# Optimization experiments

Measured on AMD Instinct MI355X. Metric: run time of the kernel, lower is better.

## Reference

```python
import jax, jax.numpy as jnp
import numpy as np

N_NODES = 50000
N_EDGES = 250000
DIMS = [300, 1024, 512, 256, 128, 2048]
NEG_SLOPE = 0.01  # F.leaky_relu default


def setup_inputs() -> dict:
    key = jax.random.key(0)
    ks = jax.random.split(key, 12)
    x = jax.random.normal(ks[0], (N_NODES, DIMS[0]), dtype=jnp.float32)
    src = jax.random.randint(ks[1], (N_EDGES,), 0, N_NODES)
    dst = jax.random.randint(ks[2], (N_EDGES,), 0, N_NODES)
    edge_index = jnp.stack([src, dst]).astype(jnp.int64)
    inp = {"x": x, "edge_index": edge_index}
    for i in range(5):
        fi, fo = DIMS[i], DIMS[i + 1]
        scale = 1.0 / np.sqrt(fi)
        inp[f"W{i+1}"] = jax.random.uniform(ks[3 + i], (fi, fo), dtype=jnp.float32, minval=-scale, maxval=scale)
        inp[f"b{i+1}"] = jnp.zeros((fo,), dtype=jnp.float32)
    return inp


def _graph_conv(x, W, b, src, dst, dinv_out, dinv_in):
    # DGL GraphConv with norm='both': D_in^{-1/2} A D_out^{-1/2} X W + b
    # per-node scalar norm commutes with the linear map, so apply W first
    # (cheaper to gather/scatter in the smaller of in/out dims; math identical)
    h = (x * dinv_out[:, None]) @ W                      # [N, out]
    agg = jax.ops.segment_sum(h[src], dst, num_segments=N_NODES)  # SpMM
    return agg * dinv_in[:, None] + b


def reference(x, edge_index, W1, b1, W2, b2, W3, b3, W4, b4, W5, b5):
    src, dst = edge_index[0], edge_index[1]
    ones = jnp.ones((N_EDGES,), dtype=x.dtype)
    out_deg = jax.ops.segment_sum(ones, src, num_segments=N_NODES)
    in_deg = jax.ops.segment_sum(ones, dst, num_segments=N_NODES)
    dinv_out = jax.lax.rsqrt(jnp.maximum(out_deg, 1.0))
    dinv_in = jax.lax.rsqrt(jnp.maximum(in_deg, 1.0))

    h = _graph_conv(x, W1, b1, src, dst, dinv_out, dinv_in)
    h = jax.nn.leaky_relu(h, NEG_SLOPE)
    h = _graph_conv(h, W2, b2, src, dst, dinv_out, dinv_in)
    h = jax.nn.leaky_relu(h, NEG_SLOPE)
    h = _graph_conv(h, W3, b3, src, dst, dinv_out, dinv_in)
    h = jax.nn.leaky_relu(h, NEG_SLOPE)
    h = _graph_conv(h, W4, b4, src, dst, dinv_out, dinv_in)
    h = jax.nn.leaky_relu(h, NEG_SLOPE)
    h = _graph_conv(h, W5, b5, src, dst, dinv_out, dinv_in)
    return h
```

## Files before the change

kernel.cpp:

```cpp
#include <hip/hip_runtime.h>

#define N_NODES 50000

typedef __attribute__((ext_vector_type(8))) short short8v;
typedef __attribute__((ext_vector_type(4))) float f32x4;
typedef unsigned int u32;
typedef unsigned short u16;

__device__ inline u16 bf16_rn(float a) {
    u32 u = __float_as_uint(a);
    return (u16)((u + 0x7FFFu + ((u >> 16) & 1u)) >> 16);
}
__device__ inline void bf16_split(float a, u16& h, u16& l) {
    h = bf16_rn(a);
    float hf = __uint_as_float(((u32)h) << 16);
    l = bf16_rn(a - hf);
}


__global__ void degree_kernel(const int* __restrict__ ei,
                              int* __restrict__ deg_out, int* __restrict__ deg_in, int E) {
    int e = blockIdx.x * blockDim.x + threadIdx.x;
    if (e >= E) return;
    int s = ei[e];
    int d = ei[E + e];
    if (s >= 0 && s < N_NODES) atomicAdd(&deg_out[s], 1);
    if (d >= 0 && d < N_NODES) atomicAdd(&deg_in[d], 1);
}

__global__ void dinv_kernel(const int* __restrict__ deg_out, const int* __restrict__ deg_in,
                            float* __restrict__ dinv_out, float* __restrict__ dinv_in, int n) {
    int v = blockIdx.x * blockDim.x + threadIdx.x;
    if (v >= n) return;
    dinv_out[v] = rsqrtf((float)max(deg_out[v], 1));
    dinv_in[v]  = rsqrtf((float)max(deg_in[v], 1));
}

__global__ void scan_kernel(const int* __restrict__ deg, int* __restrict__ row_start, int n) {
    __shared__ int sdata[1024];
    __shared__ int carry;
    int tid = threadIdx.x;
    if (tid == 0) { carry = 0; row_start[0] = 0; }
    __syncthreads();
    for (int base = 0; base < n; base += 1024) {
        int i = base + tid;
        int v = (i < n) ? deg[i] : 0;
        sdata[tid] = v;
        __syncthreads();
        for (int off = 1; off < 1024; off <<= 1) {
            int t = (tid >= off) ? sdata[tid - off] : 0;
            __syncthreads();
            sdata[tid] += t;
            __syncthreads();
        }
        if (i < n) row_start[i + 1] = carry + sdata[tid];
        __syncthreads();
        if (tid == 0) carry += sdata[1023];
        __syncthreads();
    }
}

__global__ void fill_kernel(const int* __restrict__ ei, const int* __restrict__ row_start,
                            int* __restrict__ fill_cnt, int* __restrict__ csr_src, int E) {
    int e = blockIdx.x * blockDim.x + threadIdx.x;
    if (e >= E) return;
    int s = ei[e];
    int d = ei[E + e];
    if (d < 0 || d >= N_NODES) return;
    int pos = row_start[d] + atomicAdd(&fill_cnt[d], 1);
    csr_src[pos] = s;
}


__global__ __launch_bounds__(256) void wsplit_kernel(
    const float* __restrict__ W, u16* __restrict__ Thi, u16* __restrict__ Tlo,
    int K, int Kp, int N)
{
    __shared__ float Ts[32][73];
    int tid = threadIdx.x;
    int k0 = blockIdx.x * 32, n0 = blockIdx.y * 64;
    int kk = tid >> 3, nn = (tid & 7) * 8;
    float4 v0 = make_float4(0.f, 0.f, 0.f, 0.f), v1 = v0;
    if (k0 + kk < K) {
        const float* p = W + (size_t)(k0 + kk) * N + n0 + nn;
        v0 = *reinterpret_cast<const float4*>(p);
        v1 = *reinterpret_cast<const float4*>(p + 4);
    }
    Ts[kk][nn + 0] = v0.x; Ts[kk][nn + 1] = v0.y; Ts[kk][nn + 2] = v0.z; Ts[kk][nn + 3] = v0.w;
    Ts[kk][nn + 4] = v1.x; Ts[kk][nn + 5] = v1.y; Ts[kk][nn + 6] = v1.z; Ts[kk][nn + 7] = v1.w;
    __syncthreads();
    int n = tid >> 2, kq = (tid & 3) * 8;
    union { u16 a[8]; uint4 q; } Uh, Ul;
    #pragma unroll
    for (int e = 0; e < 8; ++e) {
        u16 h, l;
        bf16_split(Ts[kq + e][n], h, l);
        Uh.a[e] = h; Ul.a[e] = l;
    }
    size_t off = (size_t)(n0 + n) * Kp + k0 + kq;
    *reinterpret_cast<uint4*>(Thi + off) = Uh.q;
    *reinterpret_cast<uint4*>(Tlo + off) = Ul.q;
}

template <bool WEIGH>
__global__ void spmm_pre_split(
    const float* __restrict__ X, const int* __restrict__ row_start,
    const int* __restrict__ csr_src,
    const float* __restrict__ dinv_out, const float* __restrict__ dinv_in,
    u16* __restrict__ Ohi, u16* __restrict__ Olo, int fo, int fopad)
{
    int v = blockIdx.x;
    int col = blockIdx.y * blockDim.x + threadIdx.x;
    if (col >= fopad) return;
    size_t o = (size_t)v * fopad + col;
    if (col >= fo) { Ohi[o] = 0; Olo[o] = 0; return; }
    int s = row_start[v], e = row_start[v + 1];
    float acc = 0.f;
    for (int i = s; i < e; ++i) {
        int u = csr_src[i];
        float h = X[(size_t)u * fo + col];
        if (WEIGH) h *= dinv_out[u];
        acc += h;
    }
    float r = acc * dinv_in[v];
    u16 hh, ll;
    bf16_split(r, hh, ll);
    Ohi[o] = hh; Olo[o] = ll;
}

template <bool SPLIT>
__global__ void spmm_post(
    const float* __restrict__ T, const int* __restrict__ row_start,
    const int* __restrict__ csr_src,
    const float* __restrict__ dinv_in, const float* __restrict__ dinv_out,
    const float* __restrict__ bias,
    u16* __restrict__ Ohi, u16* __restrict__ Olo, float* __restrict__ Of, int fo)
{
    int v = blockIdx.x;
    int col = blockIdx.y * blockDim.x + threadIdx.x;
    if (col >= fo) return;
    int s = row_start[v], e = row_start[v + 1];
    float acc = 0.f;
    for (int i = s; i < e; ++i) {
        int u = csr_src[i];
        acc += T[(size_t)u * fo + col];
    }
    float r = acc * dinv_in[v] + bias[col];
    r = (r > 0.f) ? r : 0.01f * r;
    r *= dinv_out[v];
    size_t o = (size_t)v * fo + col;
    if (SPLIT) {
        u16 hh, ll;
        bf16_split(r, hh, ll);
        Ohi[o] = hh; Olo[o] = ll;
    } else {
        Of[o] = r;
    }
}


template <bool SPLIT_OUT>
__global__ __launch_bounds__(256) void gemm_bf3_kernel(
    const u16* __restrict__ Ahi, const u16* __restrict__ Alo,
    const u16* __restrict__ Bhi, const u16* __restrict__ Blo,
    const float* __restrict__ bias, const float* __restrict__ dfold, int relu,
    u16* __restrict__ Ohi, u16* __restrict__ Olo, float* __restrict__ Of,
    int M, int Ka, int N)
{
    __shared__ u32 lds[10240];
    u32* sAh = lds;
    u32* sAl = lds + 2560;
    u32* sBh = lds + 5120;
    u32* sBl = lds + 7680;

    int tid = threadIdx.x;
    int lane = tid & 63, wave = tid >> 6;
    int wr = (wave >> 1) * 64, wc = (wave & 1) * 64;
    int bm = blockIdx.x * 128, bn = blockIdx.y * 128;

    f32x4 acc[4][4];
    #pragma unroll
    for (int i = 0; i < 4; ++i)
        #pragma unroll
        for (int j = 0; j < 4; ++j)
            acc[i][j] = (f32x4){0.f, 0.f, 0.f, 0.f};

    int sm = tid & 127, shf = tid >> 7;
    int gr = bm + sm;
    bool aok = (gr < M);
    const u16* pAh = Ahi + (size_t)(aok ? gr : 0) * Ka + shf * 16;
    const u16* pAl = Alo + (size_t)(aok ? gr : 0) * Ka + shf * 16;
    const u16* pBh = Bhi + (size_t)(bn + sm) * Ka + shf * 16;
    const u16* pBl = Blo + (size_t)(bn + sm) * Ka + shf * 16;
    int wbase = sm * 20 + shf * 8;

    int lr = lane & 15, lk = (lane >> 4) * 4;

    int nsteps = Ka >> 5;
    for (int kt = 0; kt < nsteps; ++kt) {
        size_t ko = (size_t)kt * 32;
        uint4 z = make_uint4(0, 0, 0, 0);
        uint4 vah0 = z, vah1 = z, val0 = z, val1 = z;
        if (aok) {
            vah0 = *reinterpret_cast<const uint4*>(pAh + ko);
            vah1 = *reinterpret_cast<const uint4*>(pAh + ko + 8);
            val0 = *reinterpret_cast<const uint4*>(pAl + ko);
            val1 = *reinterpret_cast<const uint4*>(pAl + ko + 8);
        }
        uint4 vbh0 = *reinterpret_cast<const uint4*>(pBh + ko);
        uint4 vbh1 = *reinterpret_cast<const uint4*>(pBh + ko + 8);
        uint4 vbl0 = *reinterpret_cast<const uint4*>(pBl + ko);
        uint4 vbl1 = *reinterpret_cast<const uint4*>(pBl + ko + 8);

        __syncthreads();
        *reinterpret_cast<uint4*>(&sAh[wbase])     = vah0;
        *reinterpret_cast<uint4*>(&sAh[wbase + 4]) = vah1;
        *reinterpret_cast<uint4*>(&sAl[wbase])     = val0;
        *reinterpret_cast<uint4*>(&sAl[wbase + 4]) = val1;
        *reinterpret_cast<uint4*>(&sBh[wbase])     = vbh0;
        *reinterpret_cast<uint4*>(&sBh[wbase + 4]) = vbh1;
        *reinterpret_cast<uint4*>(&sBl[wbase])     = vbl0;
        *reinterpret_cast<uint4*>(&sBl[wbase + 4]) = vbl1;
        __syncthreads();

        short8v ah[4], al[4], bh[4], bl[4];
        #pragma unroll
        for (int t = 0; t < 4; ++t) {
            ah[t] = *reinterpret_cast<const short8v*>(&sAh[(wr + t * 16 + lr) * 20 + lk]);
            al[t] = *reinterpret_cast<const short8v*>(&sAl[(wr + t * 16 + lr) * 20 + lk]);
            bh[t] = *reinterpret_cast<const short8v*>(&sBh[(wc + t * 16 + lr) * 20 + lk]);
            bl[t] = *reinterpret_cast<const short8v*>(&sBl[(wc + t * 16 + lr) * 20 + lk]);
        }
        #pragma unroll
        for (int i = 0; i < 4; ++i)
            #pragma unroll
            for (int j = 0; j < 4; ++j) {
                acc[i][j] = __builtin_amdgcn_mfma_f32_16x16x32_bf16(ah[i], bh[j], acc[i][j], 0, 0, 0);
                acc[i][j] = __builtin_amdgcn_mfma_f32_16x16x32_bf16(ah[i], bl[j], acc[i][j], 0, 0, 0);
                acc[i][j] = __builtin_amdgcn_mfma_f32_16x16x32_bf16(al[i], bh[j], acc[i][j], 0, 0, 0);
            }
    }

    int lq = (lane >> 4) * 4;
    float bj[4] = {0.f, 0.f, 0.f, 0.f};
    if (bias) {
        #pragma unroll
        for (int j = 0; j < 4; ++j) bj[j] = bias[bn + wc + j * 16 + lr];
    }
    #pragma unroll
    for (int i = 0; i < 4; ++i) {
        #pragma unroll
        for (int r = 0; r < 4; ++r) {
            int row = bm + wr + i * 16 + lq + r;
            if (row < M) {
                float df = 1.f;
                if (SPLIT_OUT) df = dfold[row];
                #pragma unroll
                for (int j = 0; j < 4; ++j) {
                    float v = acc[i][j][r] + bj[j];
                    if (relu) v = (v > 0.f) ? v : 0.01f * v;
                    int col = bn + wc + j * 16 + lr;
                    size_t o = (size_t)row * N + col;
                    if (SPLIT_OUT) {
                        v *= df;
                        u16 hh, ll;
                        bf16_split(v, hh, ll);
                        Ohi[o] = hh; Olo[o] = ll;
                    } else {
                        Of[o] = v;
                    }
                }
            }
        }
    }
}


extern "C" void kernel_launch(void* const* d_in, const int* in_sizes, int n_in,
                              void* d_out, int out_size, void* d_ws, size_t ws_size,
                              hipStream_t stream) {
    const float* x = (const float*)d_in[0];
    const int* ei = (const int*)d_in[1];
    const float* Wm[5] = {(const float*)d_in[2], (const float*)d_in[4], (const float*)d_in[6],
                          (const float*)d_in[8], (const float*)d_in[10]};
    const float* bv[5] = {(const float*)d_in[3], (const float*)d_in[5], (const float*)d_in[7],
                          (const float*)d_in[9], (const float*)d_in[11]};
    const int E = in_sizes[1] / 2;
    const int M = N_NODES;
    float* out = (float*)d_out;

    const int dims[6] = {300, 1024, 512, 256, 128, 2048};
    const int Kp[5]   = {320, 1024, 512, 256, 128};

    int* wsi = (int*)d_ws;
    int* deg_out   = wsi + 0;
    int* deg_in    = wsi + 50048;
    int* fill_cnt  = wsi + 100096;
    int* row_start = wsi + 150144;
    int* csr_src   = wsi + 200256;
    float* dinv_out = (float*)(wsi + 450304);
    float* dinv_in  = (float*)(wsi + 500352);
    u16* WtH = (u16*)((char*)d_ws + ((size_t)4 << 20));
    u16* WtL = (u16*)((char*)d_ws + ((size_t)7 << 20));
    u16* Xs5h = (u16*)((char*)d_ws + ((size_t)16 << 20));
    u16* Xs5l = Xs5h + (size_t)M * 128;

    size_t wtoff[6];
    wtoff[0] = 0;
    for (int l = 0; l < 5; ++l) wtoff[l + 1] = wtoff[l] + (size_t)dims[l + 1] * Kp[l];

    float* Bhalf = out + (size_t)M * 1024;
    u16* h1h = (u16*)out;               u16* h1l = h1h + (size_t)M * 1024;
    float* t2 = Bhalf;
    u16* h2h = (u16*)out;               u16* h2l = h2h + (size_t)M * 512;
    float* t3 = Bhalf;
    u16* h3h = (u16*)out;               u16* h3l = h3h + (size_t)M * 256;
    float* t4 = Bhalf;
    float* h4f = out;
    u16* Xs1h = (u16*)Bhalf;            u16* Xs1l = Xs1h + (size_t)M * 320;

    hipMemsetAsync(d_ws, 0, (size_t)150144 * 4, stream);

    degree_kernel<<<(E + 255) / 256, 256, 0, stream>>>(ei, deg_out, deg_in, E);
    dinv_kernel<<<(M + 255) / 256, 256, 0, stream>>>(deg_out, deg_in, dinv_out, dinv_in, M);
    scan_kernel<<<1, 1024, 0, stream>>>(deg_in, row_start, M);
    fill_kernel<<<(E + 255) / 256, 256, 0, stream>>>(ei, row_start, fill_cnt, csr_src, E);

    for (int l = 0; l < 5; ++l) {
        dim3 g(Kp[l] / 32, dims[l + 1] / 64);
        wsplit_kernel<<<g, 256, 0, stream>>>(Wm[l], WtH + wtoff[l], WtL + wtoff[l],
                                             dims[l], Kp[l], dims[l + 1]);
    }

    const int MB = (M + 127) / 128;

    spmm_pre_split<true><<<dim3(M, 2), 256, 0, stream>>>(x, row_start, csr_src,
        dinv_out, dinv_in, Xs1h, Xs1l, 300, 320);
    gemm_bf3_kernel<true><<<dim3(MB, 8), 256, 0, stream>>>(
        Xs1h, Xs1l, WtH + wtoff[0], WtL + wtoff[0],
        bv[0], dinv_out, 1, h1h, h1l, nullptr, M, 320, 1024);

    gemm_bf3_kernel<false><<<dim3(MB, 4), 256, 0, stream>>>(
        h1h, h1l, WtH + wtoff[1], WtL + wtoff[1],
        nullptr, nullptr, 0, nullptr, nullptr, t2, M, 1024, 512);
    spmm_post<true><<<dim3(M, 2), 256, 0, stream>>>(t2, row_start, csr_src,
        dinv_in, dinv_out, bv[1], h2h, h2l, nullptr, 512);

    gemm_bf3_kernel<false><<<dim3(MB, 2), 256, 0, stream>>>(
        h2h, h2l, WtH + wtoff[2], WtL + wtoff[2],
        nullptr, nullptr, 0, nullptr, nullptr, t3, M, 512, 256);
    spmm_post<true><<<dim3(M, 1), 256, 0, stream>>>(t3, row_start, csr_src,
        dinv_in, dinv_out, bv[2], h3h, h3l, nullptr, 256);

    gemm_bf3_kernel<false><<<dim3(MB, 1), 256, 0, stream>>>(
        h3h, h3l, WtH + wtoff[3], WtL + wtoff[3],
        nullptr, nullptr, 0, nullptr, nullptr, t4, M, 256, 128);
    spmm_post<false><<<dim3(M, 1), 128, 0, stream>>>(t4, row_start, csr_src,
        dinv_in, dinv_out, bv[3], nullptr, nullptr, h4f, 128);

    spmm_pre_split<false><<<dim3(M, 1), 128, 0, stream>>>(h4f, row_start, csr_src,
        nullptr, dinv_in, Xs5h, Xs5l, 128, 128);
    gemm_bf3_kernel<false><<<dim3(MB, 16), 256, 0, stream>>>(
        Xs5h, Xs5l, WtH + wtoff[4], WtL + wtoff[4],
        bv[4], nullptr, 0, nullptr, nullptr, out, M, 128, 2048);
}
```

Before: 1.697 ms.

## Vectorize SpMM kernels to float4 and use direct-to-LDS loads with XCD swizzle in GEMM

The SpMM gather kernels now handle four columns per thread with float4 loads and ushort4 stores, using a flat 1D grid instead of one block per node. The GEMM now stages tiles with global_load_lds straight into unpadded LDS, remaps workgroups across the 8 XCDs for L2 locality, and groups the three split-bf16 MFMA passes into separate loops. The aim is fewer memory instructions, less register staging and better cache reuse. The cost is possible LDS bank conflicts from dropping the padding and an extra barrier pattern with no double buffering.

```diff
diff --git a/kernel.cpp b/kernel.cpp
--- a/kernel.cpp
+++ b/kernel.cpp
@@ -6,6 +6,10 @@
 typedef __attribute__((ext_vector_type(4))) float f32x4;
 typedef unsigned int u32;
 typedef unsigned short u16;
+
+typedef const __attribute__((address_space(1))) void* gas_t;
+typedef __attribute__((address_space(3))) void* sas_t;
+#define GLOAD16(g, l) __builtin_amdgcn_global_load_lds((gas_t)(g), (sas_t)(l), 16, 0, 0)
 
 __device__ inline u16 bf16_rn(float a) {
     u32 u = __float_as_uint(a);
@@ -103,58 +107,77 @@
 }
 
 template <bool WEIGH>
-__global__ void spmm_pre_split(
+__global__ __launch_bounds__(256) void spmm_pre_split4(
     const float* __restrict__ X, const int* __restrict__ row_start,
     const int* __restrict__ csr_src,
     const float* __restrict__ dinv_out, const float* __restrict__ dinv_in,
-    u16* __restrict__ Ohi, u16* __restrict__ Olo, int fo, int fopad)
+    u16* __restrict__ Ohi, u16* __restrict__ Olo, int fo4, int fo4a, int total)
 {
-    int v = blockIdx.x;
-    int col = blockIdx.y * blockDim.x + threadIdx.x;
-    if (col >= fopad) return;
-    size_t o = (size_t)v * fopad + col;
-    if (col >= fo) { Ohi[o] = 0; Olo[o] = 0; return; }
+    int gid = blockIdx.x * blockDim.x + threadIdx.x;
+    if (gid >= total) return;
+    int v = gid / fo4a, c4 = gid - v * fo4a;
+    size_t o = (size_t)v * fo4a + c4;
+    ushort4* OH = (ushort4*)Ohi;
+    ushort4* OL = (ushort4*)Olo;
+    if (c4 >= fo4) {
+        ushort4 z = {0, 0, 0, 0};
+        OH[o] = z; OL[o] = z;
+        return;
+    }
     int s = row_start[v], e = row_start[v + 1];
-    float acc = 0.f;
+    const float4* X4 = (const float4*)X;
+    float4 acc = make_float4(0.f, 0.f, 0.f, 0.f);
     for (int i = s; i < e; ++i) {
         int u = csr_src[i];
-        float h = X[(size_t)u * fo + col];
-        if (WEIGH) h *= dinv_out[u];
-        acc += h;
-    }
-    float r = acc * dinv_in[v];
-    u16 hh, ll;
-    bf16_split(r, hh, ll);
-    Ohi[o] = hh; Olo[o] = ll;
+        float4 h = X4[(size_t)u * fo4 + c4];
+        float w = WEIGH ? dinv_out[u] : 1.f;
+        acc.x += h.x * w; acc.y += h.y * w; acc.z += h.z * w; acc.w += h.w * w;
+    }
+    float di = dinv_in[v];
+    float r[4] = {acc.x * di, acc.y * di, acc.z * di, acc.w * di};
+    ushort4 hh, ll;
+    bf16_split(r[0], hh.x, ll.x); bf16_split(r[1], hh.y, ll.y);
+    bf16_split(r[2], hh.z, ll.z); bf16_split(r[3], hh.w, ll.w);
+    OH[o] = hh; OL[o] = ll;
 }
 
 template <bool SPLIT>
-__global__ void spmm_post(
+__global__ __launch_bounds__(256) void spmm_post4(
     const float* __restrict__ T, const int* __restrict__ row_start,
     const int* __restrict__ csr_src,
     const float* __restrict__ dinv_in, const float* __restrict__ dinv_out,
     const float* __restrict__ bias,
-    u16* __restrict__ Ohi, u16* __restrict__ Olo, float* __restrict__ Of, int fo)
+    u16* __restrict__ Ohi, u16* __restrict__ Olo, float* __restrict__ Of,
+    int fo4, int total)
 {
-    int v = blockIdx.x;
-    int col = blockIdx.y * blockDim.x + threadIdx.x;
-    if (col >= fo) return;
+    int gid = blockIdx.x * blockDim.x + threadIdx.x;
+    if (gid >= total) return;
+    int v = gid / fo4, c4 = gid - v * fo4;
     int s = row_start[v], e = row_start[v + 1];
-    float acc = 0.f;
+    const float4* T4 = (const float4*)T;
+    float4 acc = make_float4(0.f, 0.f, 0.f, 0.f);
     for (int i = s; i < e; ++i) {
         int u = csr_src[i];
-        acc += T[(size_t)u * fo + col];
-    }
-    float r = acc * dinv_in[v] + bias[col];
-    r = (r > 0.f) ? r : 0.01f * r;
-    r *= dinv_out[v];
-    size_t o = (size_t)v * fo + col;
+        float4 h = T4[(size_t)u * fo4 + c4];
+        acc.x += h.x; acc.y += h.y; acc.z += h.z; acc.w += h.w;
+    }
+    float di = dinv_in[v], dfold = dinv_out[v];
+    float4 b4 = ((const float4*)bias)[c4];
+    float r[4] = {acc.x * di + b4.x, acc.y * di + b4.y,
+                  acc.z * di + b4.z, acc.w * di + b4.w};
+    #pragma unroll
+    for (int j = 0; j < 4; ++j) {
+        r[j] = (r[j] > 0.f) ? r[j] : 0.01f * r[j];
+        r[j] *= dfold;
+    }
+    size_t o = (size_t)v * fo4 + c4;
     if (SPLIT) {
-        u16 hh, ll;
-        bf16_split(r, hh, ll);
-        Ohi[o] = hh; Olo[o] = ll;
+        ushort4 hh, ll;
+        bf16_split(r[0], hh.x, ll.x); bf16_split(r[1], hh.y, ll.y);
+        bf16_split(r[2], hh.z, ll.z); bf16_split(r[3], hh.w, ll.w);
+        ((ushort4*)Ohi)[o] = hh; ((ushort4*)Olo)[o] = ll;
     } else {
-        Of[o] = r;
+        ((float4*)Of)[o] = make_float4(r[0], r[1], r[2], r[3]);
     }
 }
 
@@ -167,16 +190,23 @@
     u16* __restrict__ Ohi, u16* __restrict__ Olo, float* __restrict__ Of,
     int M, int Ka, int N)
 {
-    __shared__ u32 lds[10240];
-    u32* sAh = lds;
-    u32* sAl = lds + 2560;
-    u32* sBh = lds + 5120;
-    u32* sBl = lds + 7680;
+    __shared__ u16 sAh[128 * 32];
+    __shared__ u16 sAl[128 * 32];
+    __shared__ u16 sBh[128 * 32];
+    __shared__ u16 sBl[128 * 32];
 
     int tid = threadIdx.x;
     int lane = tid & 63, wave = tid >> 6;
+
+    int GY = gridDim.y;
+    int nwg = gridDim.x * GY;
+    int f = blockIdx.x * GY + blockIdx.y;
+    int q = nwg >> 3, r = nwg & 7;
+    int xcd = f & 7, idx = f >> 3;
+    int swz = (xcd < r ? xcd * (q + 1) : r * (q + 1) + (xcd - r) * q) + idx;
+    int bm = (swz / GY) * 128, bn = (swz % GY) * 128;
+
     int wr = (wave >> 1) * 64, wc = (wave & 1) * 64;
-    int bm = blockIdx.x * 128, bn = blockIdx.y * 128;
 
     f32x4 acc[4][4];
     #pragma unroll
@@ -185,60 +215,54 @@
         for (int j = 0; j < 4; ++j)
             acc[i][j] = (f32x4){0.f, 0.f, 0.f, 0.f};
 
-    int sm = tid & 127, shf = tid >> 7;
-    int gr = bm + sm;
-    bool aok = (gr < M);
-    const u16* pAh = Ahi + (size_t)(aok ? gr : 0) * Ka + shf * 16;
-    const u16* pAl = Alo + (size_t)(aok ? gr : 0) * Ka + shf * 16;
-    const u16* pBh = Bhi + (size_t)(bn + sm) * Ka + shf * 16;
-    const u16* pBl = Blo + (size_t)(bn + sm) * Ka + shf * 16;
-    int wbase = sm * 20 + shf * 8;
-
-    int lr = lane & 15, lk = (lane >> 4) * 4;
+    int rl = lane >> 2;
+    int qq = lane & 3;
+    int lr = lane & 15, lkb = (lane >> 4) * 8;
 
     int nsteps = Ka >> 5;
     for (int kt = 0; kt < nsteps; ++kt) {
-        size_t ko = (size_t)kt * 32;
-        uint4 z = make_uint4(0, 0, 0, 0);
-        uint4 vah0 = z, vah1 = z, val0 = z, val1 = z;
-        if (aok) {
-            vah0 = *reinterpret_cast<const uint4*>(pAh + ko);
-            vah1 = *reinterpret_cast<const uint4*>(pAh + ko + 8);
-            val0 = *reinterpret_cast<const uint4*>(pAl + ko);
-            val1 = *reinterpret_cast<const uint4*>(pAl + ko + 8);
+        int kb = kt * 32;
+        __syncthreads();
+        #pragma unroll
+        for (int c = 0; c < 2; ++c) {
+            int row128 = wave * 32 + c * 16 + rl;
+            int grA = min(bm + row128, M - 1);
+            int grB = bn + row128;
+            size_t aoff = (size_t)grA * Ka + kb + qq * 8;
+            size_t boff = (size_t)grB * Ka + kb + qq * 8;
+            int lb = (wave * 2 + c) * 512;
+            GLOAD16(Ahi + aoff, sAh + lb);
+            GLOAD16(Alo + aoff, sAl + lb);
+            GLOAD16(Bhi + boff, sBh + lb);
+            GLOAD16(Blo + boff, sBl + lb);
         }
-        uint4 vbh0 = *reinterpret_cast<const uint4*>(pBh + ko);
-        uint4 vbh1 = *reinterpret_cast<const uint4*>(pBh + ko + 8);
-        uint4 vbl0 = *reinterpret_cast<const uint4*>(pBl + ko);
-        uint4 vbl1 = *reinterpret_cast<const uint4*>(pBl + ko + 8);
-
         __syncthreads();
-        *reinterpret_cast<uint4*>(&sAh[wbase])     = vah0;
-        *reinterpret_cast<uint4*>(&sAh[wbase + 4]) = vah1;
-        *reinterpret_cast<uint4*>(&sAl[wbase])     = val0;
-        *reinterpret_cast<uint4*>(&sAl[wbase + 4]) = val1;
-        *reinterpret_cast<uint4*>(&sBh[wbase])     = vbh0;
-        *reinterpret_cast<uint4*>(&sBh[wbase + 4]) = vbh1;
-        *reinterpret_cast<uint4*>(&sBl[wbase])     = vbl0;
-        *reinterpret_cast<uint4*>(&sBl[wbase + 4]) = vbl1;
-        __syncthreads();
 
         short8v ah[4], al[4], bh[4], bl[4];
         #pragma unroll
         for (int t = 0; t < 4; ++t) {
-            ah[t] = *reinterpret_cast<const short8v*>(&sAh[(wr + t * 16 + lr) * 20 + lk]);
-            al[t] = *reinterpret_cast<const short8v*>(&sAl[(wr + t * 16 + lr) * 20 + lk]);
-            bh[t] = *reinterpret_cast<const short8v*>(&sBh[(wc + t * 16 + lr) * 20 + lk]);
-            bl[t] = *reinterpret_cast<const short8v*>(&sBl[(wc + t * 16 + lr) * 20 + lk]);
+            int ra = (wr + t * 16 + lr) * 32 + lkb;
+            int rb = (wc + t * 16 + lr) * 32 + lkb;
+            ah[t] = *reinterpret_cast<const short8v*>(&sAh[ra]);
+            al[t] = *reinterpret_cast<const short8v*>(&sAl[ra]);
+            bh[t] = *reinterpret_cast<const short8v*>(&sBh[rb]);
+            bl[t] = *reinterpret_cast<const short8v*>(&sBl[rb]);
         }
         #pragma unroll
         for (int i = 0; i < 4; ++i)
             #pragma unroll
-            for (int j = 0; j < 4; ++j) {
+            for (int j = 0; j < 4; ++j)
                 acc[i][j] = __builtin_amdgcn_mfma_f32_16x16x32_bf16(ah[i], bh[j], acc[i][j], 0, 0, 0);
+        #pragma unroll
+        for (int i = 0; i < 4; ++i)
+            #pragma unroll
+            for (int j = 0; j < 4; ++j)
                 acc[i][j] = __builtin_amdgcn_mfma_f32_16x16x32_bf16(ah[i], bl[j], acc[i][j], 0, 0, 0);
+        #pragma unroll
+        for (int i = 0; i < 4; ++i)
+            #pragma unroll
+            for (int j = 0; j < 4; ++j)
                 acc[i][j] = __builtin_amdgcn_mfma_f32_16x16x32_bf16(al[i], bh[j], acc[i][j], 0, 0, 0);
-            }
     }
 
     int lq = (lane >> 4) * 4;
@@ -250,14 +274,14 @@
     #pragma unroll
     for (int i = 0; i < 4; ++i) {
         #pragma unroll
-        for (int r = 0; r < 4; ++r) {
-            int row = bm + wr + i * 16 + lq + r;
+        for (int rr = 0; rr < 4; ++rr) {
+            int row = bm + wr + i * 16 + lq + rr;
             if (row < M) {
                 float df = 1.f;
                 if (SPLIT_OUT) df = dfold[row];
                 #pragma unroll
                 for (int j = 0; j < 4; ++j) {
-                    float v = acc[i][j][r] + bj[j];
+                    float v = acc[i][j][rr] + bj[j];
                     if (relu) v = (v > 0.f) ? v : 0.01f * v;
                     int col = bn + wc + j * 16 + lr;
                     size_t o = (size_t)row * N + col;
@@ -334,33 +358,44 @@
 
     const int MB = (M + 127) / 128;
 
-    spmm_pre_split<true><<<dim3(M, 2), 256, 0, stream>>>(x, row_start, csr_src,
-        dinv_out, dinv_in, Xs1h, Xs1l, 300, 320);
-    gemm_bf3_kernel<true><<<dim3(MB, 8), 256, 0, stream>>>(
-        Xs1h, Xs1l, WtH + wtoff[0], WtL + wtoff[0],
-        bv[0], dinv_out, 1, h1h, h1l, nullptr, M, 320, 1024);
-
+    {
+        int total = M * 80;
+        spmm_pre_split4<true><<<(total + 255) / 256, 256, 0, stream>>>(
+            x, row_start, csr_src, dinv_out, dinv_in, Xs1h, Xs1l, 75, 80, total);
+        gemm_bf3_kernel<true><<<dim3(MB, 8), 256, 0, stream>>>(
+            Xs1h, Xs1l, WtH + wtoff[0], WtL + wtoff[0],
+            bv[0], dinv_out, 1, h1h, h1l, nullptr, M, 320, 1024);
+    }
     gemm_bf3_kernel<false><<<dim3(MB, 4), 256, 0, stream>>>(
         h1h, h1l, WtH + wtoff[1], WtL + wtoff[1],
         nullptr, nullptr, 0, nullptr, nullptr, t2, M, 1024, 512);
-    spmm_post<true><<<dim3(M, 2), 256, 0, stream>>>(t2, row_start, csr_src,
-        dinv_in, dinv_out, bv[1], h2h, h2l, nullptr, 512);
-
+    {
+        int total = M * 128;
+        spmm_post4<true><<<(total + 255) / 256, 256, 0, stream>>>(
+            t2, row_start, csr_src, dinv_in, dinv_out, bv[1], h2h, h2l, nullptr, 128, total);
+    }
     gemm_bf3_kernel<false><<<dim3(MB, 2), 256, 0, stream>>>(
         h2h, h2l, WtH + wtoff[2], WtL + wtoff[2],
         nullptr, nullptr, 0, nullptr, nullptr, t3, M, 512, 256);
-    spmm_post<true><<<dim3(M, 1), 256, 0, stream>>>(t3, row_start, csr_src,
-        dinv_in, dinv_out, bv[2], h3h, h3l, nullptr, 256);
-
+    {
+        int total = M * 64;
+        spmm_post4<true><<<(total + 255) / 256, 256, 0, stream>>>(
+            t3, row_start, csr_src, dinv_in, dinv_out, bv[2], h3h, h3l, nullptr, 64, total);
+    }
     gemm_bf3_kernel<false><<<dim3(MB, 1), 256, 0, stream>>>(
         h3h, h3l, WtH + wtoff[3], WtL + wtoff[3],
         nullptr, nullptr, 0, nullptr, nullptr, t4, M, 256, 128);
-    spmm_post<false><<<dim3(M, 1), 128, 0, stream>>>(t4, row_start, csr_src,
-        dinv_in, dinv_out, bv[3], nullptr, nullptr, h4f, 128);
-
-    spmm_pre_split<false><<<dim3(M, 1), 128, 0, stream>>>(h4f, row_start, csr_src,
-        nullptr, dinv_in, Xs5h, Xs5l, 128, 128);
-    gemm_bf3_kernel<false><<<dim3(MB, 16), 256, 0, stream>>>(
-        Xs5h, Xs5l, WtH + wtoff[4], WtL + wtoff[4],
-        bv[4], nullptr, 0, nullptr, nullptr, out, M, 128, 2048);
-}
+    {
+        int total = M * 32;
+        spmm_post4<false><<<(total + 255) / 256, 256, 0, stream>>>(
+            t4, row_start, csr_src, dinv_in, dinv_out, bv[3], nullptr, nullptr, h4f, 32, total);
+    }
+    {
+        int total = M * 32;
+        spmm_pre_split4<false><<<(total + 255) / 256, 256, 0, stream>>>(
+            h4f, row_start, csr_src, nullptr, dinv_in, Xs5h, Xs5l, 32, 32, total);
+        gemm_bf3_kernel<false><<<dim3(MB, 16), 256, 0, stream>>>(
+            Xs5h, Xs5l, WtH + wtoff[4], WtL + wtoff[4],
+            bv[4], nullptr, 0, nullptr, nullptr, out, M, 128, 2048);
+    }
+}
```

Result: faster. 1.394 ms (-17.9%).
